# Performance work log

Measured on AMD Instinct MI355X. Metric: run time of the kernel, lower is better.

## Reference

```python
import jax, jax.numpy as jnp
import numpy as np


def setup_inputs() -> dict:
    key = jax.random.key(0)
    k1, k2, k3 = jax.random.split(key, 3)
    N, M, D, C = 4096, 8192, 1024, 128
    x = jax.random.normal(k1, (N, D), dtype=jnp.float32)
    x_n = jax.random.normal(k2, (M, D), dtype=jnp.float32)
    y = jax.random.uniform(k3, (M, C), dtype=jnp.float32)
    # module parameter: log_T = log(init_temperature) = log(1.0) = 0.0
    log_T = jnp.array(0.0, dtype=jnp.float32)
    return {"x": x, "x_n": x_n, "y": y, "log_T": log_T}


def reference(x, x_n, y, log_T):
    # Faithful to NONA.forward with similarity='euclidean', batch_norm=None,
    # agg=None, and x != x_n (plain softmax branch, no diagonal mask).
    T = jnp.exp(log_T)  # computed in the original forward but never applied
    del T
    # sim = -cdist(x, x_n, p=2)  via the ||a-b||^2 = ||a||^2 + ||b||^2 - 2ab expansion
    x_sq = jnp.sum(x * x, axis=1, keepdims=True)          # [N, 1]
    xn_sq = jnp.sum(x_n * x_n, axis=1)                    # [M]
    d2 = x_sq + xn_sq[None, :] - 2.0 * (x @ x_n.T)        # [N, M]
    sim = -jnp.sqrt(jnp.maximum(d2, 0.0))                 # [N, M]
    sim_scores = jax.nn.softmax(sim, axis=1)              # [N, M]
    return sim_scores @ y                                 # [N, C]
```

## Files before the change

kernel.cpp:

```cpp
#include <hip/hip_runtime.h>


#define N_ 4096
#define M_ 8192
#define D_ 1024
#define C_ 128
#define SPLIT 16
#define MCOLS (M_ / SPLIT)
#define NBN (MCOLS / 128)

typedef __bf16 bf16;
typedef __attribute__((ext_vector_type(8))) __bf16 bf16x8;
typedef __attribute__((ext_vector_type(4))) __bf16 bf16x4;
typedef __attribute__((ext_vector_type(4))) float f32x4;

__device__ __forceinline__ void async_copy16(const bf16* gp, void* lp) {
  __builtin_amdgcn_global_load_lds(
      (__attribute__((address_space(1))) void*)const_cast<bf16*>(gp),
      (__attribute__((address_space(3))) void*)lp, 16, 0, 0);
}

__device__ __forceinline__ int swz(int row, int gran) {
  return (row << 7) + ((gran ^ (row & 7)) << 4);
}
__device__ __forceinline__ int swz2(int row, int gran) {
  return (row << 8) + ((gran ^ (row & 15)) << 4);
}

__device__ __forceinline__ void stageA(const bf16* src, char* lds, int tid) {
  const int lane = tid & 63, wave = tid >> 6;
#pragma unroll
  for (int j = 0; j < 4; ++j) {
    const int ch  = j * 8 + wave;
    const int off = ch * 1024 + lane * 16;
    const int row = off >> 7;
    const int gr  = ((off >> 4) & 7) ^ (row & 7);
    async_copy16(src + (size_t)row * D_ + gr * 8, lds + ch * 1024);
  }
}
__device__ __forceinline__ void stageB(const bf16* src, char* lds, int tid) {
  const int lane = tid & 63, wave = tid >> 6;
#pragma unroll
  for (int j = 0; j < 2; ++j) {
    const int ch  = j * 8 + wave;
    const int off = ch * 1024 + lane * 16;
    const int row = off >> 7;
    const int gr  = ((off >> 4) & 7) ^ (row & 7);
    async_copy16(src + (size_t)row * D_ + gr * 8, lds + ch * 1024);
  }
}
__device__ __forceinline__ void stageV(const bf16* yT, int colbase, char* lds, int tid) {
  const int lane = tid & 63, wave = tid >> 6;
#pragma unroll
  for (int j = 0; j < 4; ++j) {
    const int ch  = j * 8 + wave;
    const int off = ch * 1024 + lane * 16;
    const int row = off >> 8;
    const int gr  = ((off >> 4) & 15) ^ (row & 15);
    async_copy16(yT + (size_t)row * M_ + colbase + gr * 8, lds + ch * 1024);
  }
}

#define KSTEP(Ac, Bc, DOSTG, KKP2, An, Bn, VM)                                 \
  asm volatile("s_waitcnt vmcnt(" #VM ")" ::: "memory");                       \
  __builtin_amdgcn_s_barrier();                                                \
  __builtin_amdgcn_sched_barrier(0);                                           \
  if (DOSTG) { stageA(xA + (KKP2) * 64, An, tid);                              \
               stageB(xB + (KKP2) * 64, Bn, tid); }                            \
  {                                                                            \
    _Pragma("unroll") for (int ks = 0; ks < 2; ++ks) {                         \
      bf16x8 af[4], bv[4];                                                     \
      _Pragma("unroll") for (int i = 0; i < 4; ++i)                            \
        af[i] = *(const bf16x8*)((Ac) + swz(wr * 64 + i * 16 + c, ks * 4 + g));\
      _Pragma("unroll") for (int j = 0; j < 4; ++j)                            \
        bv[j] = *(const bf16x8*)((Bc) + swz(wc * 64 + j * 16 + c, ks * 4 + g));\
      __builtin_amdgcn_s_setprio(1);                                           \
      _Pragma("unroll") for (int j = 0; j < 4; ++j)                            \
      _Pragma("unroll") for (int i = 0; i < 4; ++i)                            \
        Sacc[i][j] = __builtin_amdgcn_mfma_f32_16x16x32_bf16(                  \
            bv[j], af[i], Sacc[i][j], 0, 0, 0);                                \
      __builtin_amdgcn_s_setprio(0);                                           \
    }                                                                          \
  }

__global__ __launch_bounds__(512, 1)
void nona_main(const bf16* __restrict__ xb, const bf16* __restrict__ xnb,
               const bf16* __restrict__ yT, const float* __restrict__ xsq,
               const float* __restrict__ xnsq, float* __restrict__ Opart,
               float* __restrict__ Lpart)
{
  __shared__ __align__(16) char Lds[147456];
  char* const A0 = Lds;
  char* const A1 = Lds + 32768;
  char* const A2 = Lds + 65536;
  char* const B0 = Lds + 98304;
  char* const B1 = Lds + 114688;
  char* const B2 = Lds + 131072;
  char* const Pb = A0;
  char* const Vb = B0;

  const int tid  = threadIdx.x;
  const int lane = tid & 63;
  const int wave = tid >> 6;
  const int wr = wave & 3, wc = wave >> 2;
  const int g = lane >> 4, c = lane & 15;

  const int s    = blockIdx.x & 15;
  const int rb   = blockIdx.x >> 4;
  const int row0 = rb * 256;
  const int col0 = s * MCOLS;

  const bf16* xA = xb + (size_t)row0 * D_;

  float xs[4];
#pragma unroll
  for (int rf = 0; rf < 4; ++rf)
    xs[rf] = xsq[row0 + wr * 64 + rf * 16 + c];

  f32x4 Oacc[4][4];
  const f32x4 zero = {0.f, 0.f, 0.f, 0.f};
#pragma unroll
  for (int rf = 0; rf < 4; ++rf)
#pragma unroll
    for (int cc = 0; cc < 4; ++cc) Oacc[rf][cc] = zero;
  float lsum[4] = {0.f, 0.f, 0.f, 0.f};

#pragma unroll 1
  for (int bn = 0; bn < NBN; ++bn) {
    const int colbase = col0 + bn * 128;
    const bf16* xB = xnb + (size_t)colbase * D_;

    f32x4 Sacc[4][4];
#pragma unroll
    for (int rf = 0; rf < 4; ++rf)
#pragma unroll
      for (int cf = 0; cf < 4; ++cf) Sacc[rf][cf] = zero;

    stageA(xA, A0, tid);          stageB(xB, B0, tid);
    stageA(xA + 64, A1, tid);     stageB(xB + 64, B1, tid);

#pragma unroll 1
    for (int t = 0; t < 4; ++t) {
      const int kk = 3 * t;
      KSTEP(A0, B0, 1, kk + 2, A2, B2, 6)
      KSTEP(A1, B1, 1, kk + 3, A0, B0, 6)
      KSTEP(A2, B2, 1, kk + 4, A1, B1, 6)
    }
    KSTEP(A0, B0, 1, 14, A2, B2, 6)
    KSTEP(A1, B1, 1, 15, A0, B0, 6)
    KSTEP(A2, B2, 0, 0, A0, B0, 6)
    KSTEP(A0, B0, 0, 0, A0, B0, 0)
    __syncthreads();

    stageV(yT, colbase, Vb, tid);

#pragma unroll
    for (int cf = 0; cf < 4; ++cf) {
      const float4 nsq4 = *(const float4*)(xnsq + colbase + wc * 64 + cf * 16 + g * 4);
#pragma unroll
      for (int rf = 0; rf < 4; ++rf)
#pragma unroll
        for (int r = 0; r < 4; ++r) {
          float d2 = xs[rf] + ((const float*)&nsq4)[r] - 2.0f * Sacc[rf][cf][r];
          d2 = fmaxf(d2, 0.0f);
          const float wv = __expf(-sqrtf(d2));
          lsum[rf] += wv;
          Sacc[rf][cf][r] = wv;
        }
    }

#pragma unroll
    for (int rf = 0; rf < 4; ++rf)
#pragma unroll
      for (int cf = 0; cf < 4; ++cf) {
        bf16x4 pk;
#pragma unroll
        for (int r = 0; r < 4; ++r) pk[r] = (bf16)Sacc[rf][cf][r];
        const int row  = wr * 64 + rf * 16 + c;
        const int gran = wc * 8 + cf * 2 + (g >> 1);
        *(bf16x4*)(Pb + (row << 8) + ((gran ^ (row & 15)) << 4) + (g & 1) * 8) = pk;
      }
    __syncthreads();

#pragma unroll
    for (int ks = 0; ks < 4; ++ks) {
      bf16x8 pa[4];
#pragma unroll
      for (int rf = 0; rf < 4; ++rf)
        pa[rf] = *(const bf16x8*)(Pb + swz2(wr * 64 + rf * 16 + c, ks * 4 + g));
      __builtin_amdgcn_s_setprio(1);
#pragma unroll
      for (int cc = 0; cc < 4; ++cc) {
        bf16x8 vb = *(const bf16x8*)(Vb + swz2(wc * 64 + cc * 16 + c, ks * 4 + g));
#pragma unroll
        for (int rf = 0; rf < 4; ++rf)
          Oacc[rf][cc] = __builtin_amdgcn_mfma_f32_16x16x32_bf16(pa[rf], vb, Oacc[rf][cc], 0, 0, 0);
      }
      __builtin_amdgcn_s_setprio(0);
    }
    __syncthreads();
  }

  float* Lr = (float*)Lds;
#pragma unroll
  for (int rf = 0; rf < 4; ++rf) {
    float v = lsum[rf];
    v += __shfl_xor(v, 16);
    v += __shfl_xor(v, 32);
    if (g == 0) Lr[wc * 256 + wr * 64 + rf * 16 + c] = v;
  }
  __syncthreads();
  if (tid < 256)
    Lpart[(size_t)s * N_ + row0 + tid] = Lr[tid] + Lr[256 + tid];

  float* ob = Opart + ((size_t)s * N_ + row0) * C_;
#pragma unroll
  for (int rf = 0; rf < 4; ++rf)
#pragma unroll
    for (int cc = 0; cc < 4; ++cc)
#pragma unroll
      for (int r = 0; r < 4; ++r)
        ob[(wr * 64 + rf * 16 + g * 4 + r) * C_ + wc * 64 + cc * 16 + c] = Oacc[rf][cc][r];
}

__global__ void prep_rows(const float* __restrict__ x, const float* __restrict__ xn,
                          bf16* __restrict__ xb, bf16* __restrict__ xnb,
                          float* __restrict__ xsq, float* __restrict__ xnsq)
{
  const int blk = blockIdx.x;
  const float* src; bf16* dst; float* sq; int row;
  if (blk < N_) { src = x;  dst = xb;  sq = xsq;  row = blk; }
  else          { src = xn; dst = xnb; sq = xnsq; row = blk - N_; }
  const int t = threadIdx.x;
  const float4 v = reinterpret_cast<const float4*>(src + (size_t)row * D_)[t];
  float ss = v.x * v.x + v.y * v.y + v.z * v.z + v.w * v.w;
  bf16x4 hv;
  hv[0] = (bf16)v.x; hv[1] = (bf16)v.y; hv[2] = (bf16)v.z; hv[3] = (bf16)v.w;
  *reinterpret_cast<bf16x4*>(dst + (size_t)row * D_ + t * 4) = hv;
#pragma unroll
  for (int o = 32; o > 0; o >>= 1) ss += __shfl_down(ss, o);
  __shared__ float red[4];
  if ((t & 63) == 0) red[t >> 6] = ss;
  __syncthreads();
  if (t == 0) sq[row] = red[0] + red[1] + red[2] + red[3];
}

__global__ void prep_yT(const float* __restrict__ y, bf16* __restrict__ yT)
{
  __shared__ bf16 tile[C_][72];
  const int m0 = blockIdx.x * 64;
  const int t = threadIdx.x;
#pragma unroll
  for (int i = 0; i < 32; ++i) {
    const int idx = i * 256 + t;
    const int ml = idx >> 7, cc = idx & 127;
    tile[cc][ml] = (bf16)y[(size_t)(m0 + ml) * C_ + cc];
  }
  __syncthreads();
#pragma unroll
  for (int i = 0; i < 32; ++i) {
    const int idx = i * 256 + t;
    const int cc = idx >> 6, ml = idx & 63;
    yT[(size_t)cc * M_ + m0 + ml] = tile[cc][ml];
  }
}

__global__ void combine(const float* __restrict__ Opart, const float* __restrict__ Lpart,
                        float* __restrict__ out)
{
  const int i = blockIdx.x * 256 + threadIdx.x;
  const int row = i >> 7;
  float o = 0.f, l = 0.f;
#pragma unroll
  for (int s = 0; s < SPLIT; ++s) {
    o += Opart[(size_t)s * N_ * C_ + i];
    l += Lpart[(size_t)s * N_ + row];
  }
  out[i] = o / l;
}

extern "C" void kernel_launch(void* const* d_in, const int* in_sizes, int n_in,
                              void* d_out, int out_size, void* d_ws, size_t ws_size,
                              hipStream_t stream)
{
  const float* x  = (const float*)d_in[0];
  const float* xn = (const float*)d_in[1];
  const float* y  = (const float*)d_in[2];
  float* out = (float*)d_out;

  char* ws = (char*)d_ws;
  bf16*  xb    = (bf16*)(ws);
  bf16*  xnb   = (bf16*)(ws + (size_t)8  * 1024 * 1024);
  bf16*  yT    = (bf16*)(ws + (size_t)24 * 1024 * 1024);
  float* xsq   = (float*)(ws + (size_t)26 * 1024 * 1024);
  float* xnsq  = (float*)(ws + (size_t)26 * 1024 * 1024 + 16 * 1024);
  float* Lpart = (float*)(ws + (size_t)26 * 1024 * 1024 + 64 * 1024);
  float* Opart = (float*)(ws + (size_t)27 * 1024 * 1024);

  prep_rows<<<N_ + M_, 256, 0, stream>>>(x, xn, xb, xnb, xsq, xnsq);
  prep_yT<<<M_ / 64, 256, 0, stream>>>(y, yT);
  nona_main<<<16 * SPLIT, 512, 0, stream>>>(xb, xnb, yT, xsq, xnsq, Opart, Lpart);
  combine<<<(N_ * C_) / 256, 256, 0, stream>>>(Opart, Lpart, out);
}
```

Baseline: 150.9 us.

## Split GEMM k-steps into two phases interleaving staging with MFMA

Restructures the QK-style GEMM main loop so each 64-wide k-step runs as two phases. Each phase loads LDS fragments, issues half of the next tile's async global-to-LDS copies, then executes MFMAs between explicit barriers. The aim is to spread global load issue across the compute and overlap LDS reads, copies and MFMA more evenly, in the style of a ping-pong schedule. The cost is twice as many barriers per k-step, and the vmcnt accounting becomes more fragile.

After: 153.1 us. Within noise of the previous version (+1.4%).

```diff
diff --git a/kernel.cpp b/kernel.cpp
--- a/kernel.cpp
+++ b/kernel.cpp
@@ -27,10 +27,10 @@
   return (row << 8) + ((gran ^ (row & 15)) << 4);
 }
 
-__device__ __forceinline__ void stageA(const bf16* src, char* lds, int tid) {
+__device__ __forceinline__ void stageA_h(const bf16* src, char* lds, int tid, int j0) {
   const int lane = tid & 63, wave = tid >> 6;
 #pragma unroll
-  for (int j = 0; j < 4; ++j) {
+  for (int j = j0; j < j0 + 2; ++j) {
     const int ch  = j * 8 + wave;
     const int off = ch * 1024 + lane * 16;
     const int row = off >> 7;
@@ -38,16 +38,19 @@
     async_copy16(src + (size_t)row * D_ + gr * 8, lds + ch * 1024);
   }
 }
+__device__ __forceinline__ void stageB_h(const bf16* src, char* lds, int tid, int j) {
+  const int lane = tid & 63, wave = tid >> 6;
+  const int ch  = j * 8 + wave;
+  const int off = ch * 1024 + lane * 16;
+  const int row = off >> 7;
+  const int gr  = ((off >> 4) & 7) ^ (row & 7);
+  async_copy16(src + (size_t)row * D_ + gr * 8, lds + ch * 1024);
+}
+__device__ __forceinline__ void stageA(const bf16* src, char* lds, int tid) {
+  stageA_h(src, lds, tid, 0); stageA_h(src, lds, tid, 2);
+}
 __device__ __forceinline__ void stageB(const bf16* src, char* lds, int tid) {
-  const int lane = tid & 63, wave = tid >> 6;
-#pragma unroll
-  for (int j = 0; j < 2; ++j) {
-    const int ch  = j * 8 + wave;
-    const int off = ch * 1024 + lane * 16;
-    const int row = off >> 7;
-    const int gr  = ((off >> 4) & 7) ^ (row & 7);
-    async_copy16(src + (size_t)row * D_ + gr * 8, lds + ch * 1024);
-  }
+  stageB_h(src, lds, tid, 0); stageB_h(src, lds, tid, 1);
 }
 __device__ __forceinline__ void stageV(const bf16* yT, int colbase, char* lds, int tid) {
   const int lane = tid & 63, wave = tid >> 6;
@@ -61,27 +64,36 @@
   }
 }
 
-#define KSTEP(Ac, Bc, DOSTG, KKP2, An, Bn, VM)                                 \
-  asm volatile("s_waitcnt vmcnt(" #VM ")" ::: "memory");                       \
-  __builtin_amdgcn_s_barrier();                                                \
-  __builtin_amdgcn_sched_barrier(0);                                           \
-  if (DOSTG) { stageA(xA + (KKP2) * 64, An, tid);                              \
-               stageB(xB + (KKP2) * 64, Bn, tid); }                            \
+#define VM6  asm volatile("s_waitcnt vmcnt(6)" ::: "memory")
+#define VM0  asm volatile("s_waitcnt vmcnt(0)" ::: "memory")
+#define NOOP ((void)0)
+
+#define PHASE(Ac, Bc, KS, STG, WAIT)                                           \
   {                                                                            \
-    _Pragma("unroll") for (int ks = 0; ks < 2; ++ks) {                         \
-      bf16x8 af[4], bv[4];                                                     \
-      _Pragma("unroll") for (int i = 0; i < 4; ++i)                            \
-        af[i] = *(const bf16x8*)((Ac) + swz(wr * 64 + i * 16 + c, ks * 4 + g));\
-      _Pragma("unroll") for (int j = 0; j < 4; ++j)                            \
-        bv[j] = *(const bf16x8*)((Bc) + swz(wc * 64 + j * 16 + c, ks * 4 + g));\
-      __builtin_amdgcn_s_setprio(1);                                           \
-      _Pragma("unroll") for (int j = 0; j < 4; ++j)                            \
-      _Pragma("unroll") for (int i = 0; i < 4; ++i)                            \
-        Sacc[i][j] = __builtin_amdgcn_mfma_f32_16x16x32_bf16(                  \
-            bv[j], af[i], Sacc[i][j], 0, 0, 0);                                \
-      __builtin_amdgcn_s_setprio(0);                                           \
-    }                                                                          \
-  }
+    __builtin_amdgcn_sched_barrier(0);                                         \
+    bf16x8 af[4], bv[4];                                                       \
+    _Pragma("unroll") for (int i = 0; i < 4; ++i)                              \
+      af[i] = *(const bf16x8*)((Ac) + swz(wr * 64 + i * 16 + c, (KS) * 4 + g));\
+    _Pragma("unroll") for (int j = 0; j < 4; ++j)                              \
+      bv[j] = *(const bf16x8*)((Bc) + swz(wc * 64 + j * 16 + c, (KS) * 4 + g));\
+    STG;                                                                       \
+    WAIT;                                                                      \
+    __builtin_amdgcn_s_barrier();                                              \
+    __builtin_amdgcn_sched_barrier(0);                                         \
+    __builtin_amdgcn_s_setprio(1);                                             \
+    _Pragma("unroll") for (int j = 0; j < 4; ++j)                              \
+    _Pragma("unroll") for (int i = 0; i < 4; ++i)                              \
+      Sacc[i][j] = __builtin_amdgcn_mfma_f32_16x16x32_bf16(                    \
+          bv[j], af[i], Sacc[i][j], 0, 0, 0);                                  \
+    __builtin_amdgcn_s_setprio(0);                                             \
+    __builtin_amdgcn_s_barrier();                                              \
+  }
+
+#define KSTEP2(Ac, Bc, An, Bn, SA, SB, DO, WAIT1)                              \
+  PHASE(Ac, Bc, 0,                                                             \
+        if (DO) { stageA_h(SA, An, tid, 0); stageB_h(SB, Bn, tid, 0); }, NOOP) \
+  PHASE(Ac, Bc, 1,                                                             \
+        if (DO) { stageA_h(SA, An, tid, 2); stageB_h(SB, Bn, tid, 1); }, WAIT1)
 
 __global__ __launch_bounds__(512, 1)
 void nona_main(const bf16* __restrict__ xb, const bf16* __restrict__ xnb,
@@ -138,18 +150,21 @@
 
     stageA(xA, A0, tid);          stageB(xB, B0, tid);
     stageA(xA + 64, A1, tid);     stageB(xB + 64, B1, tid);
+    VM6;
+    __builtin_amdgcn_s_barrier();
 
 #pragma unroll 1
     for (int t = 0; t < 4; ++t) {
-      const int kk = 3 * t;
-      KSTEP(A0, B0, 1, kk + 2, A2, B2, 6)
-      KSTEP(A1, B1, 1, kk + 3, A0, B0, 6)
-      KSTEP(A2, B2, 1, kk + 4, A1, B1, 6)
+      const bf16* sa = xA + (3 * t + 2) * 64;
+      const bf16* sb = xB + (3 * t + 2) * 64;
+      KSTEP2(A0, B0, A2, B2, sa, sb, 1, VM6)
+      KSTEP2(A1, B1, A0, B0, sa + 64, sb + 64, 1, VM6)
+      KSTEP2(A2, B2, A1, B1, sa + 128, sb + 128, 1, VM6)
     }
-    KSTEP(A0, B0, 1, 14, A2, B2, 6)
-    KSTEP(A1, B1, 1, 15, A0, B0, 6)
-    KSTEP(A2, B2, 0, 0, A0, B0, 6)
-    KSTEP(A0, B0, 0, 0, A0, B0, 0)
+    KSTEP2(A0, B0, A2, B2, xA + 14 * 64, xB + 14 * 64, 1, VM6)
+    KSTEP2(A1, B1, A0, B0, xA + 15 * 64, xB + 15 * 64, 1, VM6)
+    KSTEP2(A2, B2, A0, B0, xA, xB, 0, VM0)
+    KSTEP2(A0, B0, A1, B1, xA, xB, 0, NOOP)
     __syncthreads();
 
     stageV(yT, colbase, Vb, tid);
```

## Enlarge S tile to 256x256 with double-buffered 8-phase ping-pong pipeline

Applied to the files above, without the earlier changes.

Each block now computes a 256x256 score tile per iteration instead of 256x128, with each wave owning a 128x64 sub-tile. The K loop uses two LDS buffers with a fine-grained 8-phase schedule that interleaves half-tile async loads with MFMA sub-blocks, which raises arithmetic intensity per staged byte and cuts the number of outer iterations. The P@V stage is split into two halves that reuse the freed LDS, and waves are reassigned so each one owns 32 output rows across all 128 columns. The trade-offs are higher register pressure from the 8x4 accumulator array and extra barriers per phase.

Result: slower. 177.8 us (+17.8%).

```diff
diff --git a/kernel.cpp b/kernel.cpp
--- a/kernel.cpp
+++ b/kernel.cpp
@@ -6,8 +6,7 @@
 #define D_ 1024
 #define C_ 128
 #define SPLIT 16
-#define MCOLS (M_ / SPLIT)
-#define NBN (MCOLS / 128)
+#define NIT 8
 
 typedef __bf16 bf16;
 typedef __attribute__((ext_vector_type(8))) __bf16 bf16x8;
@@ -27,18 +26,7 @@
   return (row << 8) + ((gran ^ (row & 15)) << 4);
 }
 
-__device__ __forceinline__ void stageA(const bf16* src, char* lds, int tid) {
-  const int lane = tid & 63, wave = tid >> 6;
-#pragma unroll
-  for (int j = 0; j < 4; ++j) {
-    const int ch  = j * 8 + wave;
-    const int off = ch * 1024 + lane * 16;
-    const int row = off >> 7;
-    const int gr  = ((off >> 4) & 7) ^ (row & 7);
-    async_copy16(src + (size_t)row * D_ + gr * 8, lds + ch * 1024);
-  }
-}
-__device__ __forceinline__ void stageB(const bf16* src, char* lds, int tid) {
+__device__ __forceinline__ void stageHalf(const bf16* src, char* lds, int tid) {
   const int lane = tid & 63, wave = tid >> 6;
 #pragma unroll
   for (int j = 0; j < 2; ++j) {
@@ -61,27 +49,32 @@
   }
 }
 
-#define KSTEP(Ac, Bc, DOSTG, KKP2, An, Bn, VM)                                 \
-  asm volatile("s_waitcnt vmcnt(" #VM ")" ::: "memory");                       \
+#define VM4 asm volatile("s_waitcnt vmcnt(4)" ::: "memory")
+#define VM0 asm volatile("s_waitcnt vmcnt(0)" ::: "memory")
+
+#define RD_A(AH, ABUF)                                                         \
+  _Pragma("unroll") for (int ks = 0; ks < 2; ++ks)                             \
+  _Pragma("unroll") for (int i = 0; i < 4; ++i)                                \
+    af[i][ks] = *(const bf16x8*)((ABUF) + wr * 16384 +                         \
+        swz((AH) * 64 + i * 16 + c, ks * 4 + g));
+#define RD_B(BH, BBUF)                                                         \
+  _Pragma("unroll") for (int ks = 0; ks < 2; ++ks)                             \
+  _Pragma("unroll") for (int j = 0; j < 2; ++j)                                \
+    bv[j][ks] = *(const bf16x8*)((BBUF) + (wc >> 1) * 16384 +                  \
+        swz((wc & 1) * 64 + (BH) * 32 + j * 16 + c, ks * 4 + g));
+#define MM(AH, BH)                                                             \
   __builtin_amdgcn_s_barrier();                                                \
+  asm volatile("s_waitcnt lgkmcnt(0)" ::: "memory");                           \
   __builtin_amdgcn_sched_barrier(0);                                           \
-  if (DOSTG) { stageA(xA + (KKP2) * 64, An, tid);                              \
-               stageB(xB + (KKP2) * 64, Bn, tid); }                            \
-  {                                                                            \
-    _Pragma("unroll") for (int ks = 0; ks < 2; ++ks) {                         \
-      bf16x8 af[4], bv[4];                                                     \
-      _Pragma("unroll") for (int i = 0; i < 4; ++i)                            \
-        af[i] = *(const bf16x8*)((Ac) + swz(wr * 64 + i * 16 + c, ks * 4 + g));\
-      _Pragma("unroll") for (int j = 0; j < 4; ++j)                            \
-        bv[j] = *(const bf16x8*)((Bc) + swz(wc * 64 + j * 16 + c, ks * 4 + g));\
-      __builtin_amdgcn_s_setprio(1);                                           \
-      _Pragma("unroll") for (int j = 0; j < 4; ++j)                            \
-      _Pragma("unroll") for (int i = 0; i < 4; ++i)                            \
-        Sacc[i][j] = __builtin_amdgcn_mfma_f32_16x16x32_bf16(                  \
-            bv[j], af[i], Sacc[i][j], 0, 0, 0);                                \
-      __builtin_amdgcn_s_setprio(0);                                           \
-    }                                                                          \
-  }
+  __builtin_amdgcn_s_setprio(1);                                               \
+  _Pragma("unroll") for (int ks = 0; ks < 2; ++ks)                             \
+  _Pragma("unroll") for (int j = 0; j < 2; ++j)                                \
+  _Pragma("unroll") for (int i = 0; i < 4; ++i)                                \
+    Sacc[(AH) * 4 + i][(BH) * 2 + j] = __builtin_amdgcn_mfma_f32_16x16x32_bf16(\
+        bv[j][ks], af[i][ks], Sacc[(AH) * 4 + i][(BH) * 2 + j], 0, 0, 0);      \
+  __builtin_amdgcn_s_setprio(0);                                               \
+  __builtin_amdgcn_s_barrier();                                                \
+  __builtin_amdgcn_sched_barrier(0);
 
 __global__ __launch_bounds__(512, 1)
 void nona_main(const bf16* __restrict__ xb, const bf16* __restrict__ xnb,
@@ -89,138 +82,189 @@
                const float* __restrict__ xnsq, float* __restrict__ Opart,
                float* __restrict__ Lpart)
 {
-  __shared__ __align__(16) char Lds[147456];
+  __shared__ __align__(16) char Lds[131072];
   char* const A0 = Lds;
   char* const A1 = Lds + 32768;
-  char* const A2 = Lds + 65536;
-  char* const B0 = Lds + 98304;
-  char* const B1 = Lds + 114688;
-  char* const B2 = Lds + 131072;
-  char* const Pb = A0;
-  char* const Vb = B0;
+  char* const B0 = Lds + 65536;
+  char* const B1 = Lds + 98304;
+  char* const Pb = Lds;
+  char* const V0 = Lds + 65536;
+  char* const V1 = Lds + 98304;
 
   const int tid  = threadIdx.x;
   const int lane = tid & 63;
   const int wave = tid >> 6;
-  const int wr = wave & 3, wc = wave >> 2;
+  const int wr = wave >> 2, wc = wave & 3;
   const int g = lane >> 4, c = lane & 15;
 
   const int s    = blockIdx.x & 15;
   const int rb   = blockIdx.x >> 4;
   const int row0 = rb * 256;
-  const int col0 = s * MCOLS;
 
   const bf16* xA = xb + (size_t)row0 * D_;
 
-  float xs[4];
-#pragma unroll
-  for (int rf = 0; rf < 4; ++rf)
-    xs[rf] = xsq[row0 + wr * 64 + rf * 16 + c];
-
-  f32x4 Oacc[4][4];
+  f32x4 Oacc[2][8];
   const f32x4 zero = {0.f, 0.f, 0.f, 0.f};
 #pragma unroll
-  for (int rf = 0; rf < 4; ++rf)
-#pragma unroll
-    for (int cc = 0; cc < 4; ++cc) Oacc[rf][cc] = zero;
-  float lsum[4] = {0.f, 0.f, 0.f, 0.f};
+  for (int rf = 0; rf < 2; ++rf)
+#pragma unroll
+    for (int cc = 0; cc < 8; ++cc) Oacc[rf][cc] = zero;
+  float lsum[8] = {};
 
 #pragma unroll 1
-  for (int bn = 0; bn < NBN; ++bn) {
-    const int colbase = col0 + bn * 128;
+  for (int bn = 0; bn < 2; ++bn) {
+    const int colbase = s * 512 + bn * 256;
     const bf16* xB = xnb + (size_t)colbase * D_;
 
-    f32x4 Sacc[4][4];
-#pragma unroll
-    for (int rf = 0; rf < 4; ++rf)
+    f32x4 Sacc[8][4];
+#pragma unroll
+    for (int rf = 0; rf < 8; ++rf)
 #pragma unroll
       for (int cf = 0; cf < 4; ++cf) Sacc[rf][cf] = zero;
 
-    stageA(xA, A0, tid);          stageB(xB, B0, tid);
-    stageA(xA + 64, A1, tid);     stageB(xB + 64, B1, tid);
-
+    stageHalf(xA, A0, tid);
+    stageHalf(xA + 128 * D_, A0 + 16384, tid);
+    stageHalf(xB, B0, tid);
+    stageHalf(xB + 128 * D_, B0 + 16384, tid);
+    stageHalf(xA + 64, A1, tid);
+    stageHalf(xB + 64 + 128 * D_, B1 + 16384, tid);
+    VM4;
+    __builtin_amdgcn_s_barrier();
+    __builtin_amdgcn_sched_barrier(0);
+
+    bf16x8 af[4][2], bv[2][2];
 #pragma unroll 1
-    for (int t = 0; t < 4; ++t) {
-      const int kk = 3 * t;
-      KSTEP(A0, B0, 1, kk + 2, A2, B2, 6)
-      KSTEP(A1, B1, 1, kk + 3, A0, B0, 6)
-      KSTEP(A2, B2, 1, kk + 4, A1, B1, 6)
-    }
-    KSTEP(A0, B0, 1, 14, A2, B2, 6)
-    KSTEP(A1, B1, 1, 15, A0, B0, 6)
-    KSTEP(A2, B2, 0, 0, A0, B0, 6)
-    KSTEP(A0, B0, 0, 0, A0, B0, 0)
-    __syncthreads();
-
-    stageV(yT, colbase, Vb, tid);
-
-#pragma unroll
-    for (int cf = 0; cf < 4; ++cf) {
-      const float4 nsq4 = *(const float4*)(xnsq + colbase + wc * 64 + cf * 16 + g * 4);
-#pragma unroll
-      for (int rf = 0; rf < 4; ++rf)
-#pragma unroll
-        for (int r = 0; r < 4; ++r) {
-          float d2 = xs[rf] + ((const float*)&nsq4)[r] - 2.0f * Sacc[rf][cf][r];
-          d2 = fmaxf(d2, 0.0f);
-          const float wv = __expf(-sqrtf(d2));
-          lsum[rf] += wv;
-          Sacc[rf][cf][r] = wv;
-        }
-    }
-
-#pragma unroll
-    for (int rf = 0; rf < 4; ++rf)
+    for (int t = 0; t < NIT; ++t) {
+      const bool last = (t == NIT - 1);
+      const bf16* a1 = xA + (2 * t + 1) * 64;
+      const bf16* b1 = xB + (2 * t + 1) * 64;
+      const bf16* a2 = xA + (2 * t + 2) * 64;
+      const bf16* b2 = xB + (2 * t + 2) * 64;
+      const bf16* a3 = xA + (2 * t + 3) * 64;
+      const bf16* b3 = xB + (2 * t + 3) * 64;
+
+      RD_A(0, A0) RD_B(0, B0)
+      stageHalf(a1 + 128 * D_, A1 + 16384, tid);
+      stageHalf(b1, B1, tid);
+      MM(0, 0)
+      RD_B(1, B0)
+      MM(0, 1)
+      RD_A(1, A0)
+      if (!last) stageHalf(a2, A0, tid);
+      MM(1, 1)
+      RD_B(0, B0)
+      if (!last) { stageHalf(b2 + 128 * D_, B0 + 16384, tid); VM4; }
+      else VM0;
+      MM(1, 0)
+      RD_A(0, A1) RD_B(0, B1)
+      if (!last) { stageHalf(a2 + 128 * D_, A0 + 16384, tid); stageHalf(b2, B0, tid); }
+      MM(0, 0)
+      RD_B(1, B1)
+      MM(0, 1)
+      RD_A(1, A1)
+      if (!last) stageHalf(a3, A1, tid);
+      MM(1, 1)
+      RD_B(0, B1)
+      if (!last) { stageHalf(b3 + 128 * D_, B1 + 16384, tid); VM4; }
+      MM(1, 0)
+    }
+    __syncthreads();
+
+    stageV(yT, colbase, V0, tid);
+    stageV(yT, colbase + 128, V1, tid);
+
+    {
+      float xsr[8];
+#pragma unroll
+      for (int rf = 0; rf < 8; ++rf)
+        xsr[rf] = xsq[row0 + wr * 128 + rf * 16 + c];
 #pragma unroll
       for (int cf = 0; cf < 4; ++cf) {
-        bf16x4 pk;
-#pragma unroll
-        for (int r = 0; r < 4; ++r) pk[r] = (bf16)Sacc[rf][cf][r];
-        const int row  = wr * 64 + rf * 16 + c;
-        const int gran = wc * 8 + cf * 2 + (g >> 1);
-        *(bf16x4*)(Pb + (row << 8) + ((gran ^ (row & 15)) << 4) + (g & 1) * 8) = pk;
+        const float4 nsq4 = *(const float4*)(xnsq + colbase + wc * 64 + cf * 16 + g * 4);
+#pragma unroll
+        for (int rf = 0; rf < 8; ++rf)
+#pragma unroll
+          for (int r = 0; r < 4; ++r) {
+            float d2 = xsr[rf] + ((const float*)&nsq4)[r] - 2.0f * Sacc[rf][cf][r];
+            d2 = fmaxf(d2, 0.0f);
+            const float wv = __expf(-sqrtf(d2));
+            lsum[rf] += wv;
+            Sacc[rf][cf][r] = wv;
+          }
       }
-    __syncthreads();
-
+    }
+
+#define WRITEP                                                                 \
+    _Pragma("unroll") for (int rf = 0; rf < 8; ++rf)                           \
+    _Pragma("unroll") for (int cf = 0; cf < 4; ++cf) {                         \
+      bf16x4 pk;                                                               \
+      _Pragma("unroll") for (int r = 0; r < 4; ++r) pk[r] = (bf16)Sacc[rf][cf][r]; \
+      const int prow = wr * 128 + rf * 16 + c;                                 \
+      const int gran = (wc & 1) * 8 + cf * 2 + (g >> 1);                       \
+      *(bf16x4*)(Pb + (prow << 8) + ((gran ^ (prow & 15)) << 4) + (g & 1) * 8) = pk; \
+    }
+
+    if (wc < 2) { WRITEP }
+    __syncthreads();
 #pragma unroll
     for (int ks = 0; ks < 4; ++ks) {
-      bf16x8 pa[4];
-#pragma unroll
-      for (int rf = 0; rf < 4; ++rf)
-        pa[rf] = *(const bf16x8*)(Pb + swz2(wr * 64 + rf * 16 + c, ks * 4 + g));
+      bf16x8 pa[2];
+#pragma unroll
+      for (int rf = 0; rf < 2; ++rf)
+        pa[rf] = *(const bf16x8*)(Pb + swz2(wave * 32 + rf * 16 + c, ks * 4 + g));
       __builtin_amdgcn_s_setprio(1);
 #pragma unroll
-      for (int cc = 0; cc < 4; ++cc) {
-        bf16x8 vb = *(const bf16x8*)(Vb + swz2(wc * 64 + cc * 16 + c, ks * 4 + g));
-#pragma unroll
-        for (int rf = 0; rf < 4; ++rf)
+      for (int cc = 0; cc < 8; ++cc) {
+        bf16x8 vb = *(const bf16x8*)(V0 + swz2(cc * 16 + c, ks * 4 + g));
+#pragma unroll
+        for (int rf = 0; rf < 2; ++rf)
           Oacc[rf][cc] = __builtin_amdgcn_mfma_f32_16x16x32_bf16(pa[rf], vb, Oacc[rf][cc], 0, 0, 0);
       }
       __builtin_amdgcn_s_setprio(0);
     }
     __syncthreads();
+    if (wc >= 2) { WRITEP }
+    __syncthreads();
+#pragma unroll
+    for (int ks = 0; ks < 4; ++ks) {
+      bf16x8 pa[2];
+#pragma unroll
+      for (int rf = 0; rf < 2; ++rf)
+        pa[rf] = *(const bf16x8*)(Pb + swz2(wave * 32 + rf * 16 + c, ks * 4 + g));
+      __builtin_amdgcn_s_setprio(1);
+#pragma unroll
+      for (int cc = 0; cc < 8; ++cc) {
+        bf16x8 vb = *(const bf16x8*)(V1 + swz2(cc * 16 + c, ks * 4 + g));
+#pragma unroll
+        for (int rf = 0; rf < 2; ++rf)
+          Oacc[rf][cc] = __builtin_amdgcn_mfma_f32_16x16x32_bf16(pa[rf], vb, Oacc[rf][cc], 0, 0, 0);
+      }
+      __builtin_amdgcn_s_setprio(0);
+    }
+    __syncthreads();
   }
 
   float* Lr = (float*)Lds;
 #pragma unroll
-  for (int rf = 0; rf < 4; ++rf) {
+  for (int rf = 0; rf < 8; ++rf) {
     float v = lsum[rf];
     v += __shfl_xor(v, 16);
     v += __shfl_xor(v, 32);
-    if (g == 0) Lr[wc * 256 + wr * 64 + rf * 16 + c] = v;
+    if (g == 0) Lr[wc * 256 + wr * 128 + rf * 16 + c] = v;
   }
   __syncthreads();
   if (tid < 256)
-    Lpart[(size_t)s * N_ + row0 + tid] = Lr[tid] + Lr[256 + tid];
+    Lpart[(size_t)s * N_ + row0 + tid] =
+        Lr[tid] + Lr[256 + tid] + Lr[512 + tid] + Lr[768 + tid];
 
   float* ob = Opart + ((size_t)s * N_ + row0) * C_;
 #pragma unroll
-  for (int rf = 0; rf < 4; ++rf)
-#pragma unroll
-    for (int cc = 0; cc < 4; ++cc)
+  for (int rf = 0; rf < 2; ++rf)
+#pragma unroll
+    for (int cc = 0; cc < 8; ++cc)
 #pragma unroll
       for (int r = 0; r < 4; ++r)
-        ob[(wr * 64 + rf * 16 + g * 4 + r) * C_ + wc * 64 + cc * 16 + c] = Oacc[rf][cc][r];
+        ob[(wave * 32 + rf * 16 + g * 4 + r) * C_ + cc * 16 + c] = Oacc[rf][cc][r];
 }
 
 __global__ void prep_rows(const float* __restrict__ x, const float* __restrict__ xn,
```

## Halve row tile, double-buffer K loop, raise occupancy with XCD-aware block mapping

Applied to the files above, without the earlier changes.

Shrinks the per-block row tile from 256 to 128 rows, which doubles the grid to 512 blocks. LDS per block drops from 144KB to 64KB by moving from triple-buffered to double-buffered K staging, and launch bounds now allow several blocks per CU. Block indices are remapped so blocks sharing rows and column splits land on the same XCD, for better L2 reuse. The aim is to hide latency through more resident waves, at the cost of less x_n reuse per block, a shallower prefetch pipeline and an extra barrier per K step.

After: 144.4 us. 4.3% less time.

```diff
diff --git a/kernel.cpp b/kernel.cpp
--- a/kernel.cpp
+++ b/kernel.cpp
@@ -8,6 +8,7 @@
 #define SPLIT 16
 #define MCOLS (M_ / SPLIT)
 #define NBN (MCOLS / 128)
+#define NKK (D_ / 64)
 
 typedef __bf16 bf16;
 typedef __attribute__((ext_vector_type(8))) __bf16 bf16x8;
@@ -27,18 +28,7 @@
   return (row << 8) + ((gran ^ (row & 15)) << 4);
 }
 
-__device__ __forceinline__ void stageA(const bf16* src, char* lds, int tid) {
-  const int lane = tid & 63, wave = tid >> 6;
-#pragma unroll
-  for (int j = 0; j < 4; ++j) {
-    const int ch  = j * 8 + wave;
-    const int off = ch * 1024 + lane * 16;
-    const int row = off >> 7;
-    const int gr  = ((off >> 4) & 7) ^ (row & 7);
-    async_copy16(src + (size_t)row * D_ + gr * 8, lds + ch * 1024);
-  }
-}
-__device__ __forceinline__ void stageB(const bf16* src, char* lds, int tid) {
+__device__ __forceinline__ void stage16(const bf16* src, char* lds, int tid) {
   const int lane = tid & 63, wave = tid >> 6;
 #pragma unroll
   for (int j = 0; j < 2; ++j) {
@@ -61,41 +51,20 @@
   }
 }
 
-#define KSTEP(Ac, Bc, DOSTG, KKP2, An, Bn, VM)                                 \
-  asm volatile("s_waitcnt vmcnt(" #VM ")" ::: "memory");                       \
-  __builtin_amdgcn_s_barrier();                                                \
-  __builtin_amdgcn_sched_barrier(0);                                           \
-  if (DOSTG) { stageA(xA + (KKP2) * 64, An, tid);                              \
-               stageB(xB + (KKP2) * 64, Bn, tid); }                            \
-  {                                                                            \
-    _Pragma("unroll") for (int ks = 0; ks < 2; ++ks) {                         \
-      bf16x8 af[4], bv[4];                                                     \
-      _Pragma("unroll") for (int i = 0; i < 4; ++i)                            \
-        af[i] = *(const bf16x8*)((Ac) + swz(wr * 64 + i * 16 + c, ks * 4 + g));\
-      _Pragma("unroll") for (int j = 0; j < 4; ++j)                            \
-        bv[j] = *(const bf16x8*)((Bc) + swz(wc * 64 + j * 16 + c, ks * 4 + g));\
-      __builtin_amdgcn_s_setprio(1);                                           \
-      _Pragma("unroll") for (int j = 0; j < 4; ++j)                            \
-      _Pragma("unroll") for (int i = 0; i < 4; ++i)                            \
-        Sacc[i][j] = __builtin_amdgcn_mfma_f32_16x16x32_bf16(                  \
-            bv[j], af[i], Sacc[i][j], 0, 0, 0);                                \
-      __builtin_amdgcn_s_setprio(0);                                           \
-    }                                                                          \
-  }
-
-__global__ __launch_bounds__(512, 1)
+#define VM4 asm volatile("s_waitcnt vmcnt(4)" ::: "memory")
+#define VM0 asm volatile("s_waitcnt vmcnt(0)" ::: "memory")
+
+__global__ __launch_bounds__(512, 4)
 void nona_main(const bf16* __restrict__ xb, const bf16* __restrict__ xnb,
                const bf16* __restrict__ yT, const float* __restrict__ xsq,
                const float* __restrict__ xnsq, float* __restrict__ Opart,
                float* __restrict__ Lpart)
 {
-  __shared__ __align__(16) char Lds[147456];
+  __shared__ __align__(16) char Lds[65536];
   char* const A0 = Lds;
-  char* const A1 = Lds + 32768;
-  char* const A2 = Lds + 65536;
-  char* const B0 = Lds + 98304;
-  char* const B1 = Lds + 114688;
-  char* const B2 = Lds + 131072;
+  char* const A1 = Lds + 16384;
+  char* const B0 = Lds + 32768;
+  char* const B1 = Lds + 49152;
   char* const Pb = A0;
   char* const Vb = B0;
 
@@ -105,51 +74,76 @@
   const int wr = wave & 3, wc = wave >> 2;
   const int g = lane >> 4, c = lane & 15;
 
-  const int s    = blockIdx.x & 15;
-  const int rb   = blockIdx.x >> 4;
-  const int row0 = rb * 256;
+  const int xcd = blockIdx.x & 7;
+  const int idx = blockIdx.x >> 3;
+  const int rb  = ((xcd >> 2) << 4) | (idx >> 2);
+  const int s   = ((xcd & 3) << 2) | (idx & 3);
+  const int row0 = rb * 128;
   const int col0 = s * MCOLS;
 
   const bf16* xA = xb + (size_t)row0 * D_;
 
-  float xs[4];
-#pragma unroll
-  for (int rf = 0; rf < 4; ++rf)
-    xs[rf] = xsq[row0 + wr * 64 + rf * 16 + c];
-
-  f32x4 Oacc[4][4];
+  float xs[2];
+#pragma unroll
+  for (int rf = 0; rf < 2; ++rf)
+    xs[rf] = xsq[row0 + wr * 32 + rf * 16 + c];
+
+  f32x4 Oacc[2][4];
   const f32x4 zero = {0.f, 0.f, 0.f, 0.f};
 #pragma unroll
-  for (int rf = 0; rf < 4; ++rf)
+  for (int rf = 0; rf < 2; ++rf)
 #pragma unroll
     for (int cc = 0; cc < 4; ++cc) Oacc[rf][cc] = zero;
-  float lsum[4] = {0.f, 0.f, 0.f, 0.f};
+  float lsum[2] = {0.f, 0.f};
 
 #pragma unroll 1
   for (int bn = 0; bn < NBN; ++bn) {
     const int colbase = col0 + bn * 128;
     const bf16* xB = xnb + (size_t)colbase * D_;
 
-    f32x4 Sacc[4][4];
-#pragma unroll
-    for (int rf = 0; rf < 4; ++rf)
+    f32x4 Sacc[2][4];
+#pragma unroll
+    for (int rf = 0; rf < 2; ++rf)
 #pragma unroll
       for (int cf = 0; cf < 4; ++cf) Sacc[rf][cf] = zero;
 
-    stageA(xA, A0, tid);          stageB(xB, B0, tid);
-    stageA(xA + 64, A1, tid);     stageB(xB + 64, B1, tid);
+    stage16(xA, A0, tid);
+    stage16(xB, B0, tid);
 
 #pragma unroll 1
-    for (int t = 0; t < 4; ++t) {
-      const int kk = 3 * t;
-      KSTEP(A0, B0, 1, kk + 2, A2, B2, 6)
-      KSTEP(A1, B1, 1, kk + 3, A0, B0, 6)
-      KSTEP(A2, B2, 1, kk + 4, A1, B1, 6)
+    for (int kk = 0; kk < NKK; ++kk) {
+      if (kk < NKK - 1) {
+        stage16(xA + (kk + 1) * 64, (kk & 1) ? A0 : A1, tid);
+        stage16(xB + (kk + 1) * 64, (kk & 1) ? B0 : B1, tid);
+        VM4;
+      } else {
+        VM0;
+      }
+      __builtin_amdgcn_s_barrier();
+      __builtin_amdgcn_sched_barrier(0);
+      const char* Ac = (kk & 1) ? A1 : A0;
+      const char* Bc = (kk & 1) ? B1 : B0;
+#pragma unroll
+      for (int ks = 0; ks < 2; ++ks) {
+        bf16x8 af[2], bv[4];
+#pragma unroll
+        for (int rf = 0; rf < 2; ++rf)
+          af[rf] = *(const bf16x8*)(Ac + swz(wr * 32 + rf * 16 + c, ks * 4 + g));
+#pragma unroll
+        for (int j = 0; j < 4; ++j)
+          bv[j] = *(const bf16x8*)(Bc + swz(wc * 64 + j * 16 + c, ks * 4 + g));
+        __builtin_amdgcn_s_setprio(1);
+#pragma unroll
+        for (int j = 0; j < 4; ++j)
+#pragma unroll
+          for (int rf = 0; rf < 2; ++rf)
+            Sacc[rf][j] = __builtin_amdgcn_mfma_f32_16x16x32_bf16(
+                bv[j], af[rf], Sacc[rf][j], 0, 0, 0);
+        __builtin_amdgcn_s_setprio(0);
+      }
+      __builtin_amdgcn_sched_barrier(0);
+      __builtin_amdgcn_s_barrier();
     }
-    KSTEP(A0, B0, 1, 14, A2, B2, 6)
-    KSTEP(A1, B1, 1, 15, A0, B0, 6)
-    KSTEP(A2, B2, 0, 0, A0, B0, 6)
-    KSTEP(A0, B0, 0, 0, A0, B0, 0)
     __syncthreads();
 
     stageV(yT, colbase, Vb, tid);
@@ -158,7 +152,7 @@
     for (int cf = 0; cf < 4; ++cf) {
       const float4 nsq4 = *(const float4*)(xnsq + colbase + wc * 64 + cf * 16 + g * 4);
 #pragma unroll
-      for (int rf = 0; rf < 4; ++rf)
+      for (int rf = 0; rf < 2; ++rf)
 #pragma unroll
         for (int r = 0; r < 4; ++r) {
           float d2 = xs[rf] + ((const float*)&nsq4)[r] - 2.0f * Sacc[rf][cf][r];
@@ -170,30 +164,30 @@
     }
 
 #pragma unroll
-    for (int rf = 0; rf < 4; ++rf)
+    for (int rf = 0; rf < 2; ++rf)
 #pragma unroll
       for (int cf = 0; cf < 4; ++cf) {
         bf16x4 pk;
 #pragma unroll
         for (int r = 0; r < 4; ++r) pk[r] = (bf16)Sacc[rf][cf][r];
-        const int row  = wr * 64 + rf * 16 + c;
+        const int prow = wr * 32 + rf * 16 + c;
         const int gran = wc * 8 + cf * 2 + (g >> 1);
-        *(bf16x4*)(Pb + (row << 8) + ((gran ^ (row & 15)) << 4) + (g & 1) * 8) = pk;
+        *(bf16x4*)(Pb + (prow << 8) + ((gran ^ (prow & 15)) << 4) + (g & 1) * 8) = pk;
       }
     __syncthreads();
 
 #pragma unroll
     for (int ks = 0; ks < 4; ++ks) {
-      bf16x8 pa[4];
-#pragma unroll
-      for (int rf = 0; rf < 4; ++rf)
-        pa[rf] = *(const bf16x8*)(Pb + swz2(wr * 64 + rf * 16 + c, ks * 4 + g));
+      bf16x8 pa[2];
+#pragma unroll
+      for (int rf = 0; rf < 2; ++rf)
+        pa[rf] = *(const bf16x8*)(Pb + swz2(wr * 32 + rf * 16 + c, ks * 4 + g));
       __builtin_amdgcn_s_setprio(1);
 #pragma unroll
       for (int cc = 0; cc < 4; ++cc) {
         bf16x8 vb = *(const bf16x8*)(Vb + swz2(wc * 64 + cc * 16 + c, ks * 4 + g));
 #pragma unroll
-        for (int rf = 0; rf < 4; ++rf)
+        for (int rf = 0; rf < 2; ++rf)
           Oacc[rf][cc] = __builtin_amdgcn_mfma_f32_16x16x32_bf16(pa[rf], vb, Oacc[rf][cc], 0, 0, 0);
       }
       __builtin_amdgcn_s_setprio(0);
@@ -203,24 +197,24 @@
 
   float* Lr = (float*)Lds;
 #pragma unroll
-  for (int rf = 0; rf < 4; ++rf) {
+  for (int rf = 0; rf < 2; ++rf) {
     float v = lsum[rf];
     v += __shfl_xor(v, 16);
     v += __shfl_xor(v, 32);
-    if (g == 0) Lr[wc * 256 + wr * 64 + rf * 16 + c] = v;
+    if (g == 0) Lr[wc * 128 + wr * 32 + rf * 16 + c] = v;
   }
   __syncthreads();
-  if (tid < 256)
-    Lpart[(size_t)s * N_ + row0 + tid] = Lr[tid] + Lr[256 + tid];
+  if (tid < 128)
+    Lpart[(size_t)s * N_ + row0 + tid] = Lr[tid] + Lr[128 + tid];
 
   float* ob = Opart + ((size_t)s * N_ + row0) * C_;
 #pragma unroll
-  for (int rf = 0; rf < 4; ++rf)
+  for (int rf = 0; rf < 2; ++rf)
 #pragma unroll
     for (int cc = 0; cc < 4; ++cc)
 #pragma unroll
       for (int r = 0; r < 4; ++r)
-        ob[(wr * 64 + rf * 16 + g * 4 + r) * C_ + wc * 64 + cc * 16 + c] = Oacc[rf][cc][r];
+        ob[(wr * 32 + rf * 16 + g * 4 + r) * C_ + wc * 64 + cc * 16 + c] = Oacc[rf][cc][r];
 }
 
 __global__ void prep_rows(const float* __restrict__ x, const float* __restrict__ xn,
@@ -299,6 +293,6 @@
 
   prep_rows<<<N_ + M_, 256, 0, stream>>>(x, xn, xb, xnb, xsq, xnsq);
   prep_yT<<<M_ / 64, 256, 0, stream>>>(y, yT);
-  nona_main<<<16 * SPLIT, 512, 0, stream>>>(xb, xnb, yT, xsq, xnsq, Opart, Lpart);
+  nona_main<<<32 * SPLIT, 512, 0, stream>>>(xb, xnb, yT, xsq, xnsq, Opart, Lpart);
   combine<<<(N_ * C_) / 256, 256, 0, stream>>>(Opart, Lpart, out);
 }
```
